# Performance work log

Measured on AMD Instinct MI355X. Metric: run time of the kernel, lower is better.

Reference implementation:

```python
import jax, jax.numpy as jnp
import numpy as np

N = 262144
C = 4096  # number of clusters


def _segment_max(x, seg, num_segments):
    # global_max_pool: per-cluster max over points
    return jax.ops.segment_max(x, seg, num_segments=num_segments)


def setup_inputs() -> dict:
    key = jax.random.key(0)
    ks = jax.random.split(key, 16)

    def lin(k, fan_in, fan_out):
        bound = 1.0 / np.sqrt(fan_in)
        kw, kb = jax.random.split(k)
        W = jax.random.uniform(kw, (fan_in, fan_out), jnp.float32, -bound, bound)
        b = jax.random.uniform(kb, (fan_out,), jnp.float32, -bound, bound)
        return W, b

    relative_points = jax.random.normal(ks[0], (N, 3), jnp.float32)
    features = jax.random.normal(ks[1], (N, 64), jnp.float32)
    cluster = jax.random.randint(ks[2], (N,), 0, C, jnp.int64)

    enc_W1, enc_b1 = lin(ks[3], 3, 32)    # neighborhood encoder MLP
    enc_W2, enc_b2 = lin(ks[4], 32, 64)
    W1, b1 = lin(ks[5], 3 + 64 + 64, 128)  # fc_layers (input_size + enc_out + 3)
    W2, b2 = lin(ks[6], 128, 128)
    G1, gb1 = lin(ks[7], 128, 128)          # fc_layers_global
    G2, gb2 = lin(ks[8], 128, 256)

    return dict(relative_points=relative_points, features=features, cluster=cluster,
                enc_W1=enc_W1, enc_b1=enc_b1, enc_W2=enc_W2, enc_b2=enc_b2,
                W1=W1, b1=b1, W2=W2, b2=b2, G1=G1, gb1=gb1, G2=G2, gb2=gb2)


def reference(relative_points, features, cluster,
              enc_W1, enc_b1, enc_W2, enc_b2,
              W1, b1, W2, b2, G1, gb1, G2, gb2):
    # --- neighborhood encoder: per-point MLP then per-cluster max-pool ---
    h = jax.nn.relu(relative_points @ enc_W1 + enc_b1)          # [N, 32]
    h = jax.nn.relu(h @ enc_W2 + enc_b2)                        # [N, 64]
    neigh_enc = _segment_max(h, cluster, C)                     # [C, 64]

    # gather-by-index duplication + concat
    dup = neigh_enc[cluster]                                    # [N, 64]
    encoded = jnp.concatenate([relative_points, features, dup], axis=1)  # [N, 131]

    # local fc stack (relu, leaky=False)
    encoded = jax.nn.relu(encoded @ W1 + b1)                    # [N, 128]
    encoded = jax.nn.relu(encoded @ W2 + b2)                    # [N, 128]

    # global_max_pool (mean=False)
    encoded_global = _segment_max(encoded, cluster, C)          # [C, 128]

    # global fc stack
    encoded_global = jax.nn.relu(encoded_global @ G1 + gb1)     # [C, 128]
    encoded_global = jax.nn.relu(encoded_global @ G2 + gb2)     # [C, 256]
    return encoded_global
```

## Files before the change

### kernel.cpp

```cpp
#include <hip/hip_runtime.h>
#include <hip/hip_bf16.h>

#define NN 262144
#define CC 4096
#define NBLK 64
#define PPB (NN / NBLK)
#define NT (NN / 64)
#define SLOTS 3

typedef __attribute__((ext_vector_type(8))) short bf16x8;
typedef __attribute__((ext_vector_type(4))) float f32x4;

__device__ __forceinline__ unsigned pk2(float a, float b) {
  __hip_bfloat16 ha = __float2bfloat16(a);
  __hip_bfloat16 hb = __float2bfloat16(b);
  unsigned short ua, ub;
  __builtin_memcpy(&ua, &ha, 2);
  __builtin_memcpy(&ub, &hb, 2);
  return (unsigned)ua | ((unsigned)ub << 16);
}

__global__ __launch_bounds__(256) void k_init(
    const int* __restrict__ cluster, unsigned* __restrict__ hist2d,
    const float* __restrict__ eW2, const float* __restrict__ W1,
    const float* __restrict__ W2, unsigned* __restrict__ packE,
    unsigned* __restrict__ pack1, unsigned* __restrict__ pack2)
{
  __shared__ unsigned h[CC];
  const int t = threadIdx.x, b = blockIdx.x;
  if (b < NBLK) {
    for (int q = t; q < CC; q += 256) h[q] = 0u;
    __syncthreads();
    const int base = b * PPB;
#pragma unroll 4
    for (int k = 0; k < PPB; k += 256) atomicAdd(&h[cluster[base + k + t]], 1u);
    __syncthreads();
    for (int q = t; q < CC; q += 256) hist2d[b * CC + q] = h[q];
    return;
  }
  const int id = (b - NBLK) * 256 + t;
  if (id < 1024) {
    const int nt = id >> 8, l = (id >> 2) & 63, v = id & 3;
    const int k0 = (l >> 4) * 8 + 2 * v, col = nt * 16 + (l & 15);
    packE[id] = pk2(eW2[k0 * 64 + col], eW2[(k0 + 1) * 64 + col]);
  } else if (id < 1024 + 6144) {
    const int j = id - 1024;
    const int kk = j >> 11, nt = (j >> 8) & 7, l = (j >> 2) & 63, v = j & 3;
    const int col = nt * 16 + (l & 15);
    float vals[2];
#pragma unroll
    for (int hh = 0; hh < 2; ++hh) {
      const int k = kk * 32 + (l >> 4) * 8 + 2 * v + hh;
      vals[hh] = (k < 64) ? W1[(3 + k) * 128 + col]
               : (k < 67) ? W1[(k - 64) * 128 + col] : 0.f;
    }
    pack1[j] = pk2(vals[0], vals[1]);
  } else {
    const int j = id - (1024 + 6144);
    const int kk = j >> 11, nt = (j >> 8) & 7, l = (j >> 2) & 63, v = j & 3;
    const int col = nt * 16 + (l & 15);
    const int k0 = kk * 32 + (l >> 4) * 4 + v;
    pack2[j] = pk2(W2[k0 * 128 + col], W2[(k0 + 16) * 128 + col]);
  }
}

__global__ __launch_bounds__(256) void k_scan_a(
    const unsigned* __restrict__ hist2d, unsigned* __restrict__ base2d,
    unsigned* __restrict__ totals, float4* __restrict__ psf4)
{
  const int t = threadIdx.x, b = blockIdx.x;
  if (b < 16) {
    const int c = b * 256 + t;
    unsigned acc = 0;
#pragma unroll 4
    for (int bb = 0; bb < NBLK; ++bb) {
      const unsigned v = hist2d[bb * CC + c];
      base2d[bb * CC + c] = acc;
      acc += v;
    }
    totals[c] = acc;
  } else {
    const int zb = b - 16;
    const float4 z = {0.f, 0.f, 0.f, 0.f};
    float4* __restrict__ p = psf4 + (size_t)zb * 8192 + t;
#pragma unroll 8
    for (int q = 0; q < 32; ++q) p[q * 256] = z;
  }
}

__global__ __launch_bounds__(256) void k_scatter(
    const int* __restrict__ cluster, const unsigned* __restrict__ base2d,
    const unsigned* __restrict__ totals, unsigned* __restrict__ perm,
    unsigned* __restrict__ scid, unsigned* __restrict__ cstart_g)
{
  __shared__ unsigned cur[CC];
  __shared__ unsigned part[256];
  const int t = threadIdx.x, b = blockIdx.x;
  unsigned loc[16];
  unsigned s = 0;
#pragma unroll
  for (int q = 0; q < 16; ++q) { loc[q] = s; s += totals[t * 16 + q]; }
  part[t] = s;
  __syncthreads();
  for (int off = 1; off < 256; off <<= 1) {
    const unsigned v = (t >= off) ? part[t - off] : 0u;
    __syncthreads();
    part[t] += v;
    __syncthreads();
  }
  const unsigned baset = part[t] - s;
#pragma unroll
  for (int q = 0; q < 16; ++q) {
    const unsigned cs = baset + loc[q];
    cur[t * 16 + q] = base2d[b * CC + t * 16 + q] + cs;
    if (b == 0) cstart_g[t * 16 + q] = cs;
  }
  __syncthreads();
  const int base = b * PPB;
#pragma unroll 4
  for (int k = 0; k < PPB; k += 256) {
    const int i = base + k + t;
    const int c = cluster[i];
    const unsigned pos = atomicAdd(&cur[c], 1u);
    perm[pos] = (unsigned)i;
    scid[pos] = (unsigned)c;
  }
}

__global__ __launch_bounds__(256) void k_enc_t(
    const float* __restrict__ pts, const unsigned* __restrict__ perm,
    const unsigned* __restrict__ scid, const unsigned* __restrict__ cstart,
    const float* __restrict__ eW1, const float* __restrict__ eb1,
    const float* __restrict__ eb2, const unsigned* __restrict__ packE,
    float* __restrict__ pse)
{
  __shared__ float P4[64 * 4];
  __shared__ unsigned h1s[64 * 20];
  __shared__ int seg_r0[65];
  __shared__ int seg_cid[64];
  __shared__ int seg_j[64];
  __shared__ int nseg_s;
  const int t = threadIdx.x;
  const int lane = t & 63, w = t >> 6;
  const int g = lane >> 4, ln15 = lane & 15;
  const int b = blockIdx.x;

  if (w == 0) {
    const int cid = (int)scid[b * 64 + t];
    const bool flag = (t == 0) || ((int)scid[b * 64 + t - 1] != cid);
    const unsigned long long mask = __ballot(flag);
    const int rank = (int)__popcll(mask & ((1ull << t) - 1ull));
    if (flag) {
      seg_r0[rank] = t;
      seg_cid[rank] = cid;
      seg_j[rank] = b - (int)(cstart[cid] >> 6);
    }
    if (t == 0) {
      const int ns = (int)__popcll(mask);
      nseg_s = ns;
      seg_r0[ns] = 64;
    }
    const int i = (int)perm[b * 64 + t];
    P4[t * 4 + 0] = pts[i * 3 + 0];
    P4[t * 4 + 1] = pts[i * 3 + 1];
    P4[t * 4 + 2] = pts[i * 3 + 2];
    P4[t * 4 + 3] = 0.f;
  }
  __syncthreads();
  {
    const int r = t >> 2, qq = t & 3;
    const float p0 = P4[r * 4], p1 = P4[r * 4 + 1], p2 = P4[r * 4 + 2];
    unsigned wv[4];
#pragma unroll
    for (int u = 0; u < 4; ++u) {
      float hv[2];
#pragma unroll
      for (int hh = 0; hh < 2; ++hh) {
        const int cc2 = qq * 8 + 2 * u + hh;
        hv[hh] = fmaxf(fmaf(p2, eW1[64 + cc2],
                       fmaf(p1, eW1[32 + cc2],
                       fmaf(p0, eW1[cc2], eb1[cc2]))), 0.f);
      }
      wv[u] = pk2(hv[0], hv[1]);
    }
    uint4 st; st.x = wv[0]; st.y = wv[1]; st.z = wv[2]; st.w = wv[3];
    *reinterpret_cast<uint4*>(&h1s[r * 20 + qq * 4]) = st;
  }
  __syncthreads();
  {
    const int col = w * 16 + ln15;
    const bf16x8 bfr = *reinterpret_cast<const bf16x8*>(&packE[(w * 64 + lane) * 4]);
    const float bias = eb2[col];
    f32x4 acc[4];
#pragma unroll
    for (int m = 0; m < 4; ++m) acc[m] = f32x4{bias, bias, bias, bias};
#pragma unroll
    for (int m = 0; m < 4; ++m) {
      const bf16x8 a = *reinterpret_cast<const bf16x8*>(&h1s[(16 * m + ln15) * 20 + g * 4]);
      acc[m] = __builtin_amdgcn_mfma_f32_16x16x32_bf16(a, bfr, acc[m], 0, 0, 0);
    }
    const int nseg = nseg_s;
    for (int s = 0; s < nseg; ++s) {
      const int r0 = seg_r0[s], r1 = seg_r0[s + 1];
      float v = 0.f;
#pragma unroll
      for (int m = 0; m < 4; ++m)
#pragma unroll
        for (int q = 0; q < 4; ++q) {
          const int row = 16 * m + 4 * g + q;
          const bool in = (row >= r0) & (row < r1);
          v = fmaxf(v, in ? fmaxf(acc[m][q], 0.f) : 0.f);
        }
      v = fmaxf(v, __shfl_xor(v, 16, 64));
      v = fmaxf(v, __shfl_xor(v, 32, 64));
      if (lane < 16) {
        const int c = seg_cid[s], j = seg_j[s];
        if (j < SLOTS - 1)
          pse[((size_t)c * SLOTS + j) * 64 + col] = v;
        else
          atomicMax((int*)&pse[((size_t)c * SLOTS + (SLOTS - 1)) * 64 + col],
                    __float_as_int(v));
      }
    }
  }
}

__global__ __launch_bounds__(256) void k_cproj2(
    const float* __restrict__ pse, const float* __restrict__ W1,
    const float* __restrict__ b1, float* __restrict__ cproj)
{
  __shared__ float nm2[2][64];
  const int t = threadIdx.x, b = blockIdx.x;
  if (t < 128) {
    const int rr = t >> 6, col = t & 63;
    const float* p = pse + ((size_t)(b * 2 + rr) * SLOTS) * 64 + col;
    nm2[rr][col] = fmaxf(fmaxf(p[0], p[64]), p[128]);
  }
  __syncthreads();
  const int rr = t >> 7, col = t & 127;
  const float* __restrict__ Wd = W1 + 67 * 128;
  float a = b1[col];
#pragma unroll 4
  for (int j = 0; j < 16; ++j) {
    const f32x4 nv = *reinterpret_cast<const f32x4*>(&nm2[rr][4 * j]);
    a = fmaf(nv[0], Wd[(4 * j + 0) * 128 + col], a);
    a = fmaf(nv[1], Wd[(4 * j + 1) * 128 + col], a);
    a = fmaf(nv[2], Wd[(4 * j + 2) * 128 + col], a);
    a = fmaf(nv[3], Wd[(4 * j + 3) * 128 + col], a);
  }
  cproj[(size_t)(b * 2 + rr) * 128 + col] = a;
}

__global__ __launch_bounds__(256) void k_fc_t(
    const float* __restrict__ pts, const float* __restrict__ feat,
    const unsigned* __restrict__ perm, const unsigned* __restrict__ scid,
    const unsigned* __restrict__ cstart, const float* __restrict__ b2,
    const float* __restrict__ cproj, const unsigned* __restrict__ pack1,
    const unsigned* __restrict__ pack2, float* __restrict__ psf)
{
  __shared__ unsigned buf[64 * 68];
  __shared__ float cpd[8][128];
  __shared__ int ridx_l[64];
  __shared__ int cid_l[64];
  __shared__ int seg_r0[65];
  __shared__ int seg_cid[64];
  __shared__ int seg_j[64];
  __shared__ int nseg_s;
  const int t = threadIdx.x;
  const int lane = t & 63, w = t >> 6;
  const int g = lane >> 4, ln15 = lane & 15;
  const int b = blockIdx.x;

  if (w == 0) {
    const int cid = (int)scid[b * 64 + t];
    cid_l[t] = cid;
    const bool flag = (t == 0) || ((int)scid[b * 64 + t - 1] != cid);
    const unsigned long long mask = __ballot(flag);
    const int rank = (int)__popcll(mask & ((1ull << t) - 1ull));
    ridx_l[t] = (int)__popcll(mask & ((2ull << t) - 1ull)) - 1;
    if (flag) {
      seg_r0[rank] = t;
      seg_cid[rank] = cid;
      seg_j[rank] = b - (int)(cstart[cid] >> 6);
    }
    if (t == 0) {
      const int ns = (int)__popcll(mask);
      nseg_s = ns;
      seg_r0[ns] = 64;
    }
  }
  {
    const int r = t >> 2, seg = t & 3;
    const int i = (int)perm[b * 64 + r];
    const float4* __restrict__ fp = reinterpret_cast<const float4*>(&feat[(size_t)i * 64 + seg * 16]);
    const float4 f0 = fp[0], f1 = fp[1], f2 = fp[2], f3 = fp[3];
    uint4 s0v, s1v;
    s0v.x = pk2(f0.x, f0.y); s0v.y = pk2(f0.z, f0.w);
    s0v.z = pk2(f1.x, f1.y); s0v.w = pk2(f1.z, f1.w);
    s1v.x = pk2(f2.x, f2.y); s1v.y = pk2(f2.z, f2.w);
    s1v.z = pk2(f3.x, f3.y); s1v.w = pk2(f3.z, f3.w);
    *reinterpret_cast<uint4*>(&buf[r * 52 + seg * 8 + 0]) = s0v;
    *reinterpret_cast<uint4*>(&buf[r * 52 + seg * 8 + 4]) = s1v;
  }
  if (t < 64) {
    const int i = (int)perm[b * 64 + t];
    uint4 pw;
    pw.x = pk2(pts[i * 3 + 0], pts[i * 3 + 1]);
    pw.y = pk2(pts[i * 3 + 2], 0.f);
    pw.z = 0u; pw.w = 0u;
    uint4 zz; zz.x = zz.y = zz.z = zz.w = 0u;
    *reinterpret_cast<uint4*>(&buf[t * 52 + 32]) = pw;
    *reinterpret_cast<uint4*>(&buf[t * 52 + 36]) = zz;
    *reinterpret_cast<uint4*>(&buf[t * 52 + 40]) = zz;
    *reinterpret_cast<uint4*>(&buf[t * 52 + 44]) = zz;
  }
  __syncthreads();
  {
    const int nseg = nseg_s;
    const int lim = (nseg < 8) ? nseg : 8;
    for (int s = t >> 7; s < lim; s += 2)
      cpd[s][t & 127] = cproj[(size_t)seg_cid[s] * 128 + (t & 127)];
  }
  __syncthreads();

  const int colA = w * 32 + ln15, colB = colA + 16;
  f32x4 acc0[4], acc1[4];
  {
    const int nseg = nseg_s;
    if (nseg <= 2) {
      const float cA0 = cpd[0][colA], cA1 = cpd[0][colB];
      const float cB0 = (nseg == 2) ? cpd[1][colA] : cA0;
      const float cB1 = (nseg == 2) ? cpd[1][colB] : cA1;
      const int rb = (nseg == 2) ? seg_r0[1] : 64;
#pragma unroll
      for (int m = 0; m < 4; ++m)
#pragma unroll
        for (int q = 0; q < 4; ++q) {
          const int row = 16 * m + 4 * g + q;
          acc0[m][q] = (row < rb) ? cA0 : cB0;
          acc1[m][q] = (row < rb) ? cA1 : cB1;
        }
    } else {
#pragma unroll
      for (int m = 0; m < 4; ++m)
#pragma unroll
        for (int q = 0; q < 4; ++q) {
          const int row = 16 * m + 4 * g + q;
          const int idx = ridx_l[row];
          if (idx < 8) {
            acc0[m][q] = cpd[idx][colA];
            acc1[m][q] = cpd[idx][colB];
          } else {
            const int cc = cid_l[row];
            acc0[m][q] = cproj[(size_t)cc * 128 + colA];
            acc1[m][q] = cproj[(size_t)cc * 128 + colB];
          }
        }
    }
  }
  {
#pragma unroll
    for (int kk = 0; kk < 3; ++kk) {
      const bf16x8 bf0 = *reinterpret_cast<const bf16x8*>(&pack1[((kk * 8 + 2 * w + 0) * 64 + lane) * 4]);
      const bf16x8 bf1 = *reinterpret_cast<const bf16x8*>(&pack1[((kk * 8 + 2 * w + 1) * 64 + lane) * 4]);
#pragma unroll
      for (int m = 0; m < 4; ++m) {
        const bf16x8 a = *reinterpret_cast<const bf16x8*>(&buf[(16 * m + ln15) * 52 + kk * 16 + g * 4]);
        acc0[m] = __builtin_amdgcn_mfma_f32_16x16x32_bf16(a, bf0, acc0[m], 0, 0, 0);
        acc1[m] = __builtin_amdgcn_mfma_f32_16x16x32_bf16(a, bf1, acc1[m], 0, 0, 0);
      }
    }
  }
  __syncthreads();
  {
#pragma unroll
    for (int m = 0; m < 4; ++m)
#pragma unroll
      for (int q = 0; q < 4; ++q) {
        const int row = 16 * m + 4 * g + q;
        buf[row * 68 + w * 16 + ln15] =
            pk2(fmaxf(acc0[m][q], 0.f), fmaxf(acc1[m][q], 0.f));
      }
  }
  __syncthreads();
  {
    const float bb0 = b2[colA], bb1 = b2[colB];
#pragma unroll
    for (int m = 0; m < 4; ++m) {
      acc0[m] = f32x4{bb0, bb0, bb0, bb0};
      acc1[m] = f32x4{bb1, bb1, bb1, bb1};
    }
#pragma unroll
    for (int kk = 0; kk < 4; ++kk) {
      const bf16x8 bf0 = *reinterpret_cast<const bf16x8*>(&pack2[((kk * 8 + 2 * w + 0) * 64 + lane) * 4]);
      const bf16x8 bf1 = *reinterpret_cast<const bf16x8*>(&pack2[((kk * 8 + 2 * w + 1) * 64 + lane) * 4]);
#pragma unroll
      for (int m = 0; m < 4; ++m) {
        const bf16x8 a = *reinterpret_cast<const bf16x8*>(&buf[(16 * m + ln15) * 68 + kk * 16 + g * 4]);
        acc0[m] = __builtin_amdgcn_mfma_f32_16x16x32_bf16(a, bf0, acc0[m], 0, 0, 0);
        acc1[m] = __builtin_amdgcn_mfma_f32_16x16x32_bf16(a, bf1, acc1[m], 0, 0, 0);
      }
    }
  }
  {
    const int nseg = nseg_s;
    for (int s = 0; s < nseg; ++s) {
      const int r0 = seg_r0[s], r1 = seg_r0[s + 1];
      float v0 = 0.f, v1 = 0.f;
#pragma unroll
      for (int m = 0; m < 4; ++m)
#pragma unroll
        for (int q = 0; q < 4; ++q) {
          const int row = 16 * m + 4 * g + q;
          const bool in = (row >= r0) & (row < r1);
          v0 = fmaxf(v0, in ? fmaxf(acc0[m][q], 0.f) : 0.f);
          v1 = fmaxf(v1, in ? fmaxf(acc1[m][q], 0.f) : 0.f);
        }
      v0 = fmaxf(v0, __shfl_xor(v0, 16, 64)); v0 = fmaxf(v0, __shfl_xor(v0, 32, 64));
      v1 = fmaxf(v1, __shfl_xor(v1, 16, 64)); v1 = fmaxf(v1, __shfl_xor(v1, 32, 64));
      if (lane < 16) {
        const int c = seg_cid[s], j = seg_j[s];
        if (j < SLOTS - 1) {
          psf[((size_t)c * SLOTS + j) * 128 + colA] = v0;
          psf[((size_t)c * SLOTS + j) * 128 + colB] = v1;
        } else {
          atomicMax((int*)&psf[((size_t)c * SLOTS + (SLOTS - 1)) * 128 + colA], __float_as_int(v0));
          atomicMax((int*)&psf[((size_t)c * SLOTS + (SLOTS - 1)) * 128 + colB], __float_as_int(v1));
        }
      }
    }
  }
}

__global__ __launch_bounds__(256) void k_glob(
    const float* __restrict__ psf, const float* __restrict__ G1,
    const float* __restrict__ gb1, const float* __restrict__ G2,
    const float* __restrict__ gb2, float* __restrict__ out)
{
  __shared__ float pooled[128];
  __shared__ float part[256];
  __shared__ float tg[128];
  const int t = threadIdx.x, c = blockIdx.x;
  if (t < 128) {
    const float* p = psf + (size_t)c * SLOTS * 128 + t;
    pooled[t] = fmaxf(fmaxf(p[0], p[128]), p[256]);
  }
  __syncthreads();
  {
    const int col = t & 127, half = t >> 7;
    float a = half ? 0.f : gb1[col];
#pragma unroll 2
    for (int j = 0; j < 16; ++j) {
      const f32x4 pv = *reinterpret_cast<const f32x4*>(&pooled[half * 64 + 4 * j]);
      a = fmaf(pv[0], G1[(half * 64 + 4 * j + 0) * 128 + col], a);
      a = fmaf(pv[1], G1[(half * 64 + 4 * j + 1) * 128 + col], a);
      a = fmaf(pv[2], G1[(half * 64 + 4 * j + 2) * 128 + col], a);
      a = fmaf(pv[3], G1[(half * 64 + 4 * j + 3) * 128 + col], a);
    }
    part[t] = a;
  }
  __syncthreads();
  if (t < 128) tg[t] = fmaxf(part[t] + part[t + 128], 0.f);
  __syncthreads();
  {
    float a = gb2[t];
#pragma unroll 2
    for (int j = 0; j < 32; ++j) {
      const f32x4 tv = *reinterpret_cast<const f32x4*>(&tg[4 * j]);
      a = fmaf(tv[0], G2[(4 * j + 0) * 256 + t], a);
      a = fmaf(tv[1], G2[(4 * j + 1) * 256 + t], a);
      a = fmaf(tv[2], G2[(4 * j + 2) * 256 + t], a);
      a = fmaf(tv[3], G2[(4 * j + 3) * 256 + t], a);
    }
    out[(size_t)c * 256 + t] = fmaxf(a, 0.f);
  }
}

extern "C" void kernel_launch(void* const* d_in, const int* in_sizes, int n_in,
                              void* d_out, int out_size, void* d_ws, size_t ws_size,
                              hipStream_t stream)
{
  (void)in_sizes; (void)n_in; (void)out_size; (void)ws_size;
  const float* pts  = (const float*)d_in[0];
  const float* feat = (const float*)d_in[1];
  const int*   clus = (const int*)  d_in[2];
  const float* eW1  = (const float*)d_in[3];
  const float* eb1  = (const float*)d_in[4];
  const float* eW2  = (const float*)d_in[5];
  const float* eb2  = (const float*)d_in[6];
  const float* W1   = (const float*)d_in[7];
  const float* b1   = (const float*)d_in[8];
  const float* W2   = (const float*)d_in[9];
  const float* b2   = (const float*)d_in[10];
  const float* G1   = (const float*)d_in[11];
  const float* gb1  = (const float*)d_in[12];
  const float* G2   = (const float*)d_in[13];
  const float* gb2  = (const float*)d_in[14];
  float* out = (float*)d_out;

  unsigned* ws      = (unsigned*)d_ws;
  unsigned* hist2d  = ws;
  unsigned* base2d  = ws + 262144;
  float*    pse     = (float*)ws;
  unsigned* totals  = ws + 786432;
  unsigned* cstart  = ws + 790528;
  unsigned* perm    = ws + 794624;
  unsigned* scid    = ws + 1056768;
  unsigned* packE   = ws + 1318912;
  unsigned* pack1   = ws + 1319936;
  unsigned* pack2   = ws + 1326080;
  float*    cproj   = (float*)(ws + 1334272);
  float*    psf     = (float*)(ws + 1858560);

  k_init   <<<NBLK + 60, 256, 0, stream>>>(clus, hist2d, eW2, W1, W2,
                                           packE, pack1, pack2);
  k_scan_a <<<64, 256, 0, stream>>>(hist2d, base2d, totals, (float4*)psf);
  k_scatter<<<NBLK, 256, 0, stream>>>(clus, base2d, totals, perm, scid, cstart);
  hipMemsetAsync((void*)pse, 0, (size_t)786432 * 4, stream);
  k_enc_t  <<<NT, 256, 0, stream>>>(pts, perm, scid, cstart, eW1, eb1, eb2, packE, pse);
  k_cproj2 <<<CC / 2, 256, 0, stream>>>(pse, W1, b1, cproj);
  k_fc_t   <<<NT, 256, 0, stream>>>(pts, feat, perm, scid, cstart, b2, cproj,
                                    pack1, pack2, psf);
  k_glob   <<<CC, 256, 0, stream>>>(psf, G1, gb1, G2, gb2, out);
}
```

Measured before the change: 119.0 us.

## Fuse cluster projection into encoder, pack perm+cid, batch global MLP per block

Merges perm and cluster id into one packed word to halve index traffic. The separate cproj kernel is folded into the encoder: a per-cluster atomic tile counter lets the last tile of each cluster compute that cluster's projection. The memset is folded into the scan kernel's zeroing, and the global MLP processes 16 clusters per block so the G1/G2 weight loads are reused. The trade-offs are extra atomics, serialized per-segment work in the encoder tail, and more register pressure in k_glob.

```diff
diff --git a/kernel.cpp b/kernel.cpp
--- a/kernel.cpp
+++ b/kernel.cpp
@@ -64,9 +64,10 @@
   }
 }
 
+#define ZERO_F4 590848
 __global__ __launch_bounds__(256) void k_scan_a(
     const unsigned* __restrict__ hist2d, unsigned* __restrict__ base2d,
-    unsigned* __restrict__ totals, float4* __restrict__ psf4)
+    unsigned* __restrict__ totals, float4* __restrict__ zbase)
 {
   const int t = threadIdx.x, b = blockIdx.x;
   if (b < 16) {
@@ -82,16 +83,18 @@
   } else {
     const int zb = b - 16;
     const float4 z = {0.f, 0.f, 0.f, 0.f};
-    float4* __restrict__ p = psf4 + (size_t)zb * 8192 + t;
-#pragma unroll 8
-    for (int q = 0; q < 32; ++q) p[q * 256] = z;
+#pragma unroll 5
+    for (int q = 0; q < 25; ++q) {
+      const int idx = (zb * 25 + q) * 256 + t;
+      if (idx < ZERO_F4) zbase[idx] = z;
+    }
   }
 }
 
 __global__ __launch_bounds__(256) void k_scatter(
     const int* __restrict__ cluster, const unsigned* __restrict__ base2d,
-    const unsigned* __restrict__ totals, unsigned* __restrict__ perm,
-    unsigned* __restrict__ scid, unsigned* __restrict__ cstart_g)
+    const unsigned* __restrict__ totals, unsigned* __restrict__ permcid,
+    unsigned* __restrict__ cstart_g)
 {
   __shared__ unsigned cur[CC];
   __shared__ unsigned part[256];
@@ -122,17 +125,18 @@
     const int i = base + k + t;
     const int c = cluster[i];
     const unsigned pos = atomicAdd(&cur[c], 1u);
-    perm[pos] = (unsigned)i;
-    scid[pos] = (unsigned)c;
+    permcid[pos] = (unsigned)i | ((unsigned)c << 18);
   }
 }
 
 __global__ __launch_bounds__(256) void k_enc_t(
-    const float* __restrict__ pts, const unsigned* __restrict__ perm,
-    const unsigned* __restrict__ scid, const unsigned* __restrict__ cstart,
+    const float* __restrict__ pts, const unsigned* __restrict__ permcid,
+    const unsigned* __restrict__ cstart, const unsigned* __restrict__ totals,
     const float* __restrict__ eW1, const float* __restrict__ eb1,
     const float* __restrict__ eb2, const unsigned* __restrict__ packE,
-    float* __restrict__ pse)
+    float* __restrict__ pse, const float* __restrict__ W1,
+    const float* __restrict__ b1, unsigned* __restrict__ cntE,
+    float* __restrict__ cproj)
 {
   __shared__ float P4[64 * 4];
   __shared__ unsigned h1s[64 * 20];
@@ -140,14 +144,18 @@
   __shared__ int seg_cid[64];
   __shared__ int seg_j[64];
   __shared__ int nseg_s;
+  __shared__ float nmb[64];
+  __shared__ int finfl[64];
   const int t = threadIdx.x;
   const int lane = t & 63, w = t >> 6;
   const int g = lane >> 4, ln15 = lane & 15;
   const int b = blockIdx.x;
 
   if (w == 0) {
-    const int cid = (int)scid[b * 64 + t];
-    const bool flag = (t == 0) || ((int)scid[b * 64 + t - 1] != cid);
+    const unsigned pc = permcid[b * 64 + t];
+    const int cid = (int)(pc >> 18);
+    const int prevcid = (t == 0) ? -1 : (int)(permcid[b * 64 + t - 1] >> 18);
+    const bool flag = (t == 0) || (prevcid != cid);
     const unsigned long long mask = __ballot(flag);
     const int rank = (int)__popcll(mask & ((1ull << t) - 1ull));
     if (flag) {
@@ -160,7 +168,7 @@
       nseg_s = ns;
       seg_r0[ns] = 64;
     }
-    const int i = (int)perm[b * 64 + t];
+    const int i = (int)(pc & 0x3FFFFu);
     P4[t * 4 + 0] = pts[i * 3 + 0];
     P4[t * 4 + 1] = pts[i * 3 + 1];
     P4[t * 4 + 2] = pts[i * 3 + 2];
@@ -223,40 +231,43 @@
       }
     }
   }
-}
-
-__global__ __launch_bounds__(256) void k_cproj2(
-    const float* __restrict__ pse, const float* __restrict__ W1,
-    const float* __restrict__ b1, float* __restrict__ cproj)
-{
-  __shared__ float nm2[2][64];
-  const int t = threadIdx.x, b = blockIdx.x;
-  if (t < 128) {
-    const int rr = t >> 6, col = t & 63;
-    const float* p = pse + ((size_t)(b * 2 + rr) * SLOTS) * 64 + col;
-    nm2[rr][col] = fmaxf(fmaxf(p[0], p[64]), p[128]);
-  }
-  __syncthreads();
-  const int rr = t >> 7, col = t & 127;
-  const float* __restrict__ Wd = W1 + 67 * 128;
-  float a = b1[col];
+  __syncthreads();
+  if (t < nseg_s) {
+    const int c = seg_cid[t];
+    const int cs = (int)cstart[c];
+    const int szc = (int)totals[c];
+    const int ntil = ((cs + szc - 1) >> 6) - (cs >> 6) + 1;
+    const unsigned old = __hip_atomic_fetch_add(&cntE[c], 1u, __ATOMIC_ACQ_REL,
+                                                __HIP_MEMORY_SCOPE_AGENT);
+    finfl[t] = ((int)old + 1 == ntil) ? 1 : 0;
+  }
+  __syncthreads();
+  const int nseg2 = nseg_s;
+  for (int s = 0; s < nseg2; ++s) {
+    if (!finfl[s]) continue;
+    const int c = seg_cid[s];
+    if (t < 64) {
+      const float* p = pse + (size_t)c * (SLOTS * 64) + t;
+      nmb[t] = fmaxf(fmaxf(p[0], p[64]), p[128]);
+    }
+    __syncthreads();
+    if (t < 128) {
+      float a = b1[t];
+      const float* __restrict__ Wd = W1 + 67 * 128;
 #pragma unroll 4
-  for (int j = 0; j < 16; ++j) {
-    const f32x4 nv = *reinterpret_cast<const f32x4*>(&nm2[rr][4 * j]);
-    a = fmaf(nv[0], Wd[(4 * j + 0) * 128 + col], a);
-    a = fmaf(nv[1], Wd[(4 * j + 1) * 128 + col], a);
-    a = fmaf(nv[2], Wd[(4 * j + 2) * 128 + col], a);
-    a = fmaf(nv[3], Wd[(4 * j + 3) * 128 + col], a);
-  }
-  cproj[(size_t)(b * 2 + rr) * 128 + col] = a;
+      for (int k = 0; k < 64; ++k) a = fmaf(nmb[k], Wd[k * 128 + t], a);
+      cproj[(size_t)c * 128 + t] = a;
+    }
+    __syncthreads();
+  }
 }
 
 __global__ __launch_bounds__(256) void k_fc_t(
     const float* __restrict__ pts, const float* __restrict__ feat,
-    const unsigned* __restrict__ perm, const unsigned* __restrict__ scid,
-    const unsigned* __restrict__ cstart, const float* __restrict__ b2,
-    const float* __restrict__ cproj, const unsigned* __restrict__ pack1,
-    const unsigned* __restrict__ pack2, float* __restrict__ psf)
+    const unsigned* __restrict__ permcid, const unsigned* __restrict__ cstart,
+    const float* __restrict__ b2, const float* __restrict__ cproj,
+    const unsigned* __restrict__ pack1, const unsigned* __restrict__ pack2,
+    float* __restrict__ psf)
 {
   __shared__ unsigned buf[64 * 68];
   __shared__ float cpd[8][128];
@@ -272,9 +283,11 @@
   const int b = blockIdx.x;
 
   if (w == 0) {
-    const int cid = (int)scid[b * 64 + t];
+    const unsigned pc = permcid[b * 64 + t];
+    const int cid = (int)(pc >> 18);
     cid_l[t] = cid;
-    const bool flag = (t == 0) || ((int)scid[b * 64 + t - 1] != cid);
+    const int prevcid = (t == 0) ? -1 : (int)(permcid[b * 64 + t - 1] >> 18);
+    const bool flag = (t == 0) || (prevcid != cid);
     const unsigned long long mask = __ballot(flag);
     const int rank = (int)__popcll(mask & ((1ull << t) - 1ull));
     ridx_l[t] = (int)__popcll(mask & ((2ull << t) - 1ull)) - 1;
@@ -291,7 +304,7 @@
   }
   {
     const int r = t >> 2, seg = t & 3;
-    const int i = (int)perm[b * 64 + r];
+    const int i = (int)(permcid[b * 64 + r] & 0x3FFFFu);
     const float4* __restrict__ fp = reinterpret_cast<const float4*>(&feat[(size_t)i * 64 + seg * 16]);
     const float4 f0 = fp[0], f1 = fp[1], f2 = fp[2], f3 = fp[3];
     uint4 s0v, s1v;
@@ -303,7 +316,7 @@
     *reinterpret_cast<uint4*>(&buf[r * 52 + seg * 8 + 4]) = s1v;
   }
   if (t < 64) {
-    const int i = (int)perm[b * 64 + t];
+    const int i = (int)(permcid[b * 64 + t] & 0x3FFFFu);
     uint4 pw;
     pw.x = pk2(pts[i * 3 + 0], pts[i * 3 + 1]);
     pw.y = pk2(pts[i * 3 + 2], 0.f);
@@ -437,42 +450,46 @@
     const float* __restrict__ gb1, const float* __restrict__ G2,
     const float* __restrict__ gb2, float* __restrict__ out)
 {
-  __shared__ float pooled[128];
-  __shared__ float part[256];
-  __shared__ float tg[128];
-  const int t = threadIdx.x, c = blockIdx.x;
-  if (t < 128) {
-    const float* p = psf + (size_t)c * SLOTS * 128 + t;
-    pooled[t] = fmaxf(fmaxf(p[0], p[128]), p[256]);
-  }
-  __syncthreads();
-  {
-    const int col = t & 127, half = t >> 7;
-    float a = half ? 0.f : gb1[col];
+  __shared__ float pooled[16][128];
+  __shared__ float tg[16][128];
+  const int t = threadIdx.x, b = blockIdx.x;
+  const int c0 = b * 16;
+#pragma unroll
+  for (int q = 0; q < 8; ++q) {
+    const int idx = q * 256 + t;
+    const int cc = idx >> 7, col = idx & 127;
+    const float* p = psf + (size_t)(c0 + cc) * (SLOTS * 128) + col;
+    pooled[cc][col] = fmaxf(fmaxf(p[0], p[128]), p[256]);
+  }
+  __syncthreads();
+  {
+    const int col = t & 127, hi = t >> 7;
+    float acc[8];
+#pragma unroll
+    for (int q = 0; q < 8; ++q) acc[q] = gb1[col];
 #pragma unroll 2
-    for (int j = 0; j < 16; ++j) {
-      const f32x4 pv = *reinterpret_cast<const f32x4*>(&pooled[half * 64 + 4 * j]);
-      a = fmaf(pv[0], G1[(half * 64 + 4 * j + 0) * 128 + col], a);
-      a = fmaf(pv[1], G1[(half * 64 + 4 * j + 1) * 128 + col], a);
-      a = fmaf(pv[2], G1[(half * 64 + 4 * j + 2) * 128 + col], a);
-      a = fmaf(pv[3], G1[(half * 64 + 4 * j + 3) * 128 + col], a);
-    }
-    part[t] = a;
-  }
-  __syncthreads();
-  if (t < 128) tg[t] = fmaxf(part[t] + part[t + 128], 0.f);
-  __syncthreads();
-  {
-    float a = gb2[t];
+    for (int k = 0; k < 128; ++k) {
+      const float wv = G1[k * 128 + col];
+#pragma unroll
+      for (int q = 0; q < 8; ++q) acc[q] = fmaf(pooled[q * 2 + hi][k], wv, acc[q]);
+    }
+#pragma unroll
+    for (int q = 0; q < 8; ++q) tg[q * 2 + hi][col] = fmaxf(acc[q], 0.f);
+  }
+  __syncthreads();
+  {
+    float o[16];
+#pragma unroll
+    for (int q = 0; q < 16; ++q) o[q] = gb2[t];
 #pragma unroll 2
-    for (int j = 0; j < 32; ++j) {
-      const f32x4 tv = *reinterpret_cast<const f32x4*>(&tg[4 * j]);
-      a = fmaf(tv[0], G2[(4 * j + 0) * 256 + t], a);
-      a = fmaf(tv[1], G2[(4 * j + 1) * 256 + t], a);
-      a = fmaf(tv[2], G2[(4 * j + 2) * 256 + t], a);
-      a = fmaf(tv[3], G2[(4 * j + 3) * 256 + t], a);
-    }
-    out[(size_t)c * 256 + t] = fmaxf(a, 0.f);
+    for (int k = 0; k < 128; ++k) {
+      const float wv = G2[k * 256 + t];
+#pragma unroll
+      for (int q = 0; q < 16; ++q) o[q] = fmaf(tg[q][k], wv, o[q]);
+    }
+#pragma unroll
+    for (int q = 0; q < 16; ++q)
+      out[(size_t)(c0 + q) * 256 + t] = fmaxf(o[q], 0.f);
   }
 }
 
@@ -501,25 +518,24 @@
   unsigned* ws      = (unsigned*)d_ws;
   unsigned* hist2d  = ws;
   unsigned* base2d  = ws + 262144;
-  float*    pse     = (float*)ws;
-  unsigned* totals  = ws + 786432;
-  unsigned* cstart  = ws + 790528;
-  unsigned* perm    = ws + 794624;
-  unsigned* scid    = ws + 1056768;
-  unsigned* packE   = ws + 1318912;
-  unsigned* pack1   = ws + 1319936;
-  unsigned* pack2   = ws + 1326080;
-  float*    cproj   = (float*)(ws + 1334272);
-  float*    psf     = (float*)(ws + 1858560);
+  unsigned* totals  = ws + 524288;
+  unsigned* cstart  = ws + 528384;
+  unsigned* permcid = ws + 532480;
+  unsigned* packE   = ws + 794624;
+  unsigned* pack1   = ws + 795648;
+  unsigned* pack2   = ws + 801792;
+  float*    cproj   = (float*)(ws + 809984);
+  float*    pse     = (float*)(ws + 1334272);
+  float*    psf     = (float*)(ws + 2120704);
+  unsigned* cntE    = ws + 3693568;
 
   k_init   <<<NBLK + 60, 256, 0, stream>>>(clus, hist2d, eW2, W1, W2,
                                            packE, pack1, pack2);
-  k_scan_a <<<64, 256, 0, stream>>>(hist2d, base2d, totals, (float4*)psf);
-  k_scatter<<<NBLK, 256, 0, stream>>>(clus, base2d, totals, perm, scid, cstart);
-  hipMemsetAsync((void*)pse, 0, (size_t)786432 * 4, stream);
-  k_enc_t  <<<NT, 256, 0, stream>>>(pts, perm, scid, cstart, eW1, eb1, eb2, packE, pse);
-  k_cproj2 <<<CC / 2, 256, 0, stream>>>(pse, W1, b1, cproj);
-  k_fc_t   <<<NT, 256, 0, stream>>>(pts, feat, perm, scid, cstart, b2, cproj,
+  k_scan_a <<<112, 256, 0, stream>>>(hist2d, base2d, totals, (float4*)pse);
+  k_scatter<<<NBLK, 256, 0, stream>>>(clus, base2d, totals, permcid, cstart);
+  k_enc_t  <<<NT, 256, 0, stream>>>(pts, permcid, cstart, totals, eW1, eb1, eb2,
+                                    packE, pse, W1, b1, cntE, cproj);
+  k_fc_t   <<<NT, 256, 0, stream>>>(pts, feat, permcid, cstart, b2, cproj,
                                     pack1, pack2, psf);
-  k_glob   <<<CC, 256, 0, stream>>>(psf, G1, gb1, G2, gb2, out);
-}
+  k_glob   <<<256, 256, 0, stream>>>(psf, G1, gb1, G2, gb2, out);
+}
```

After: 207.2 us. 1.74x slower.
